# Optimization experiments

Measured on AMD Instinct MI355X. Metric: run time of the kernel, lower is better.

Reference implementation:

```python
import jax, jax.numpy as jnp
import numpy as np

B, T, C, F = 512, 1024, 8, 8
ISIZE = C * F  # 64
OSIZE = 64


def setup_inputs() -> dict:
    key = jax.random.key(0)
    k_x, k_w, k_b = jax.random.split(key, 3)
    x = jax.random.normal(k_x, (B, T, C, F), dtype=jnp.float32)
    # per-group Linear params, torch nn.Linear layout: weight [osize, isize], bias [osize]
    bound = 1.0 / np.sqrt(ISIZE)
    W = jax.random.uniform(k_w, (T, OSIZE, ISIZE), dtype=jnp.float32, minval=-bound, maxval=bound)
    b = jax.random.uniform(k_b, (T, OSIZE), dtype=jnp.float32, minval=-bound, maxval=bound)
    return {"x": x, "W": W, "b": b}


def reference(x, W, b):
    # collapseDims: cat(x.split(1, 2), 3).squeeze(2) == reshape [B,T,C,F] -> [B,T,C*F]
    Bn, Tn, Cn, Fn = x.shape
    xc = x.reshape(Bn, Tn, Cn * Fn)
    # per-slice Linear along dim=1 (T groups): y[b,t,:] = xc[b,t,:] @ W[t].T + b[t]
    out = jnp.einsum("bti,toi->bto", xc, W) + b[None, :, :]
    return out
```

## Files before the change

### kernel.cpp

```cpp
#include <hip/hip_runtime.h>


#define T_DIM 1024
#define B_DIM 512
#define KSZ 64
#define OSZ 64
#define ROWS 64

typedef __attribute__((ext_vector_type(8))) short   short8;
typedef __attribute__((ext_vector_type(8))) unsigned short ushort8;
typedef __attribute__((ext_vector_type(4))) float   f32x4;

static __device__ __forceinline__ unsigned short f2bf(float f) {
    unsigned u = __float_as_uint(f);
    u += 0x7FFFu + ((u >> 16) & 1u);
    return (unsigned short)(u >> 16);
}
static __device__ __forceinline__ float bf2f(unsigned short h) {
    return __uint_as_float((unsigned)h << 16);
}

__global__ __launch_bounds__(256, 4) void pl_kernel(
    const float* __restrict__ x,
    const float* __restrict__ W,
    const float* __restrict__ bias,
    float* __restrict__ out)
{
    __shared__ unsigned short Xh[ROWS * KSZ];
    __shared__ unsigned short Xl[ROWS * KSZ];
    __shared__ unsigned short Wh[OSZ * KSZ];
    __shared__ unsigned short Wl[OSZ * KSZ];

    const int t     = blockIdx.x >> 3;
    const int chunk = blockIdx.x & 7;
    const int row0  = chunk * ROWS;
    const int tid   = threadIdx.x;

    const int sr = tid >> 2;
    const int kc = tid & 3;

    {
        const float* xp = x + ((size_t)(row0 + sr) * T_DIM + t) * KSZ + 16 * kc;
        float4 f0 = *(const float4*)(xp);
        float4 f1 = *(const float4*)(xp + 4);
        float4 f2 = *(const float4*)(xp + 8);
        float4 f3 = *(const float4*)(xp + 12);
        float a[8]  = {f0.x, f0.y, f0.z, f0.w, f1.x, f1.y, f1.z, f1.w};
        float b2[8] = {f2.x, f2.y, f2.z, f2.w, f3.x, f3.y, f3.z, f3.w};
        ushort8 h0, l0, h1, l1;
        #pragma unroll
        for (int j = 0; j < 8; ++j) {
            unsigned short hh = f2bf(a[j]);
            h0[j] = hh; l0[j] = f2bf(a[j] - bf2f(hh));
            unsigned short h2 = f2bf(b2[j]);
            h1[j] = h2; l1[j] = f2bf(b2[j] - bf2f(h2));
        }
        const int p0 = (((2 * kc)     ^ (sr & 7)) << 3);
        const int p1 = (((2 * kc + 1) ^ (sr & 7)) << 3);
        *(ushort8*)&Xh[sr * KSZ + p0] = h0;
        *(ushort8*)&Xl[sr * KSZ + p0] = l0;
        *(ushort8*)&Xh[sr * KSZ + p1] = h1;
        *(ushort8*)&Xl[sr * KSZ + p1] = l1;
    }
    {
        const float* wp = W + (size_t)t * (OSZ * KSZ) + (size_t)sr * KSZ + 16 * kc;
        float4 f0 = *(const float4*)(wp);
        float4 f1 = *(const float4*)(wp + 4);
        float4 f2 = *(const float4*)(wp + 8);
        float4 f3 = *(const float4*)(wp + 12);
        float a[8]  = {f0.x, f0.y, f0.z, f0.w, f1.x, f1.y, f1.z, f1.w};
        float b2[8] = {f2.x, f2.y, f2.z, f2.w, f3.x, f3.y, f3.z, f3.w};
        ushort8 h0, l0, h1, l1;
        #pragma unroll
        for (int j = 0; j < 8; ++j) {
            unsigned short hh = f2bf(a[j]);
            h0[j] = hh; l0[j] = f2bf(a[j] - bf2f(hh));
            unsigned short h2 = f2bf(b2[j]);
            h1[j] = h2; l1[j] = f2bf(b2[j] - bf2f(h2));
        }
        const int p0 = (((2 * kc)     ^ (sr & 7)) << 3);
        const int p1 = (((2 * kc + 1) ^ (sr & 7)) << 3);
        *(ushort8*)&Wh[sr * KSZ + p0] = h0;
        *(ushort8*)&Wl[sr * KSZ + p0] = l0;
        *(ushort8*)&Wh[sr * KSZ + p1] = h1;
        *(ushort8*)&Wl[sr * KSZ + p1] = l1;
    }

    __syncthreads();

    const int w  = tid >> 6;
    const int l  = tid & 63;
    const int kq = l >> 4;

    const int arow = 16 * w + (l & 15);
    short8 ah[2], al[2];
    #pragma unroll
    for (int ks = 0; ks < 2; ++ks) {
        const int kb  = ks * 4 + kq;
        const int pos = (kb ^ (arow & 7)) << 3;
        ah[ks] = *(const short8*)&Xh[arow * KSZ + pos];
        al[ks] = *(const short8*)&Xl[arow * KSZ + pos];
    }

    f32x4 acc[4] = {};
    #pragma unroll
    for (int ct = 0; ct < 4; ++ct) {
        const int brow = 16 * ct + (l & 15);
        #pragma unroll
        for (int ks = 0; ks < 2; ++ks) {
            const int kb  = ks * 4 + kq;
            const int pos = (kb ^ (brow & 7)) << 3;
            short8 bh = *(const short8*)&Wh[brow * KSZ + pos];
            short8 bl = *(const short8*)&Wl[brow * KSZ + pos];
            acc[ct] = __builtin_amdgcn_mfma_f32_16x16x32_bf16(ah[ks], bh, acc[ct], 0, 0, 0);
            acc[ct] = __builtin_amdgcn_mfma_f32_16x16x32_bf16(al[ks], bh, acc[ct], 0, 0, 0);
            acc[ct] = __builtin_amdgcn_mfma_f32_16x16x32_bf16(ah[ks], bl, acc[ct], 0, 0, 0);
        }
    }

    #pragma unroll
    for (int ct = 0; ct < 4; ++ct) {
        const float bv = bias[(size_t)t * OSZ + 16 * ct + (l & 15)];
        #pragma unroll
        for (int j = 0; j < 4; ++j) {
            const size_t b = (size_t)row0 + 16 * w + 4 * kq + j;
            out[(b * T_DIM + t) * OSZ + 16 * ct + (l & 15)] = acc[ct][j] + bv;
        }
    }
}

extern "C" void kernel_launch(void* const* d_in, const int* in_sizes, int n_in,
                              void* d_out, int out_size, void* d_ws, size_t ws_size,
                              hipStream_t stream) {
    const float* x    = (const float*)d_in[0];
    const float* W    = (const float*)d_in[1];
    const float* bias = (const float*)d_in[2];
    float* out        = (float*)d_out;

    dim3 grid(T_DIM * (B_DIM / ROWS));
    dim3 block(256);
    pl_kernel<<<grid, block, 0, stream>>>(x, W, bias, out);
}
```

Before: 72.40 us.

## Process four T slices per block with register-resident weights and LDS-staged coalesced stores

Each block now handles four consecutive t values, with one wave per t. Each wave keeps its own W[t] split into bf16 hi/lo parts in registers instead of staging it in LDS. X rows for four t values are loaded as contiguous 1 KB spans per row. Outputs are staged through a padded LDS buffer so each thread writes 256 contiguous bytes, replacing the previous scattered 64-byte row stores. This improves global coalescing for the strided [B,T,...] layout, at the cost of 68 KB of LDS, lower occupancy (launch bounds 2) and more registers per thread.

```diff
diff --git a/kernel.cpp b/kernel.cpp
--- a/kernel.cpp
+++ b/kernel.cpp
@@ -6,9 +6,10 @@
 #define KSZ 64
 #define OSZ 64
 #define ROWS 64
+#define NT 4
+#define RS 272
 
 typedef __attribute__((ext_vector_type(8))) short   short8;
-typedef __attribute__((ext_vector_type(8))) unsigned short ushort8;
 typedef __attribute__((ext_vector_type(4))) float   f32x4;
 
 static __device__ __forceinline__ unsigned short f2bf(float f) {
@@ -20,112 +21,139 @@
     return __uint_as_float((unsigned)h << 16);
 }
 
-__global__ __launch_bounds__(256, 4) void pl_kernel(
+__global__ __launch_bounds__(256, 2) void pl_kernel(
     const float* __restrict__ x,
     const float* __restrict__ W,
     const float* __restrict__ bias,
     float* __restrict__ out)
 {
-    __shared__ unsigned short Xh[ROWS * KSZ];
-    __shared__ unsigned short Xl[ROWS * KSZ];
-    __shared__ unsigned short Wh[OSZ * KSZ];
-    __shared__ unsigned short Wl[OSZ * KSZ];
+    __shared__ __align__(16) unsigned char smem[69632];
+    unsigned short* Xh = (unsigned short*)smem;
+    unsigned short* Xl = (unsigned short*)(smem + 32768);
+    float* Ob = (float*)smem;
 
-    const int t     = blockIdx.x >> 3;
+    const int quad  = blockIdx.x >> 3;
     const int chunk = blockIdx.x & 7;
+    const int T0    = quad * NT;
     const int row0  = chunk * ROWS;
     const int tid   = threadIdx.x;
+    const int w     = tid >> 6;
+    const int l     = tid & 63;
+    const int n     = l & 15;
+    const int kq    = l >> 4;
 
-    const int sr = tid >> 2;
-    const int kc = tid & 3;
+    short8 wh[4][2], wl[4][2];
+    {
+        const float* wp = W + ((size_t)(T0 + w) * OSZ + n) * KSZ + kq * 8;
+        #pragma unroll
+        for (int ct = 0; ct < 4; ++ct) {
+            #pragma unroll
+            for (int ks = 0; ks < 2; ++ks) {
+                const float* p = wp + (size_t)ct * 16 * KSZ + ks * 32;
+                float4 f0 = *(const float4*)(p);
+                float4 f1 = *(const float4*)(p + 4);
+                float a[8] = {f0.x, f0.y, f0.z, f0.w, f1.x, f1.y, f1.z, f1.w};
+                short8 h, lo;
+                #pragma unroll
+                for (int j = 0; j < 8; ++j) {
+                    unsigned short hh = f2bf(a[j]);
+                    h[j]  = (short)hh;
+                    lo[j] = (short)f2bf(a[j] - bf2f(hh));
+                }
+                wh[ct][ks] = h; wl[ct][ks] = lo;
+            }
+        }
+    }
 
     {
-        const float* xp = x + ((size_t)(row0 + sr) * T_DIM + t) * KSZ + 16 * kc;
-        float4 f0 = *(const float4*)(xp);
-        float4 f1 = *(const float4*)(xp + 4);
-        float4 f2 = *(const float4*)(xp + 8);
-        float4 f3 = *(const float4*)(xp + 12);
-        float a[8]  = {f0.x, f0.y, f0.z, f0.w, f1.x, f1.y, f1.z, f1.w};
-        float b2[8] = {f2.x, f2.y, f2.z, f2.w, f3.x, f3.y, f3.z, f3.w};
-        ushort8 h0, l0, h1, l1;
+        const int sr = tid >> 2;
+        const int sq = tid & 3;
+        const float* xp = x + ((size_t)(row0 + sr) * T_DIM + (T0 + sq)) * KSZ;
+        unsigned short* xh = Xh + sq * 4096 + sr * 64;
+        unsigned short* xl = Xl + sq * 4096 + sr * 64;
+        const int swz = (sr & 7) ^ ((sq & 1) << 2);
         #pragma unroll
-        for (int j = 0; j < 8; ++j) {
-            unsigned short hh = f2bf(a[j]);
-            h0[j] = hh; l0[j] = f2bf(a[j] - bf2f(hh));
-            unsigned short h2 = f2bf(b2[j]);
-            h1[j] = h2; l1[j] = f2bf(b2[j] - bf2f(h2));
+        for (int bb = 0; bb < 4; ++bb) {
+            float4 f0 = *(const float4*)(xp + bb * 16);
+            float4 f1 = *(const float4*)(xp + bb * 16 + 4);
+            float4 f2 = *(const float4*)(xp + bb * 16 + 8);
+            float4 f3 = *(const float4*)(xp + bb * 16 + 12);
+            float a[8]  = {f0.x, f0.y, f0.z, f0.w, f1.x, f1.y, f1.z, f1.w};
+            float b2[8] = {f2.x, f2.y, f2.z, f2.w, f3.x, f3.y, f3.z, f3.w};
+            short8 h0, l0, h1, l1;
+            #pragma unroll
+            for (int j = 0; j < 8; ++j) {
+                unsigned short hh = f2bf(a[j]);
+                h0[j] = (short)hh; l0[j] = (short)f2bf(a[j] - bf2f(hh));
+                unsigned short h2 = f2bf(b2[j]);
+                h1[j] = (short)h2; l1[j] = (short)f2bf(b2[j] - bf2f(h2));
+            }
+            const int g0 = (2 * bb)     ^ swz;
+            const int g1 = (2 * bb + 1) ^ swz;
+            *(short8*)(xh + g0 * 8) = h0;
+            *(short8*)(xl + g0 * 8) = l0;
+            *(short8*)(xh + g1 * 8) = h1;
+            *(short8*)(xl + g1 * 8) = l1;
         }
-        const int p0 = (((2 * kc)     ^ (sr & 7)) << 3);
-        const int p1 = (((2 * kc + 1) ^ (sr & 7)) << 3);
-        *(ushort8*)&Xh[sr * KSZ + p0] = h0;
-        *(ushort8*)&Xl[sr * KSZ + p0] = l0;
-        *(ushort8*)&Xh[sr * KSZ + p1] = h1;
-        *(ushort8*)&Xl[sr * KSZ + p1] = l1;
-    }
-    {
-        const float* wp = W + (size_t)t * (OSZ * KSZ) + (size_t)sr * KSZ + 16 * kc;
-        float4 f0 = *(const float4*)(wp);
-        float4 f1 = *(const float4*)(wp + 4);
-        float4 f2 = *(const float4*)(wp + 8);
-        float4 f3 = *(const float4*)(wp + 12);
-        float a[8]  = {f0.x, f0.y, f0.z, f0.w, f1.x, f1.y, f1.z, f1.w};
-        float b2[8] = {f2.x, f2.y, f2.z, f2.w, f3.x, f3.y, f3.z, f3.w};
-        ushort8 h0, l0, h1, l1;
-        #pragma unroll
-        for (int j = 0; j < 8; ++j) {
-            unsigned short hh = f2bf(a[j]);
-            h0[j] = hh; l0[j] = f2bf(a[j] - bf2f(hh));
-            unsigned short h2 = f2bf(b2[j]);
-            h1[j] = h2; l1[j] = f2bf(b2[j] - bf2f(h2));
-        }
-        const int p0 = (((2 * kc)     ^ (sr & 7)) << 3);
-        const int p1 = (((2 * kc + 1) ^ (sr & 7)) << 3);
-        *(ushort8*)&Wh[sr * KSZ + p0] = h0;
-        *(ushort8*)&Wl[sr * KSZ + p0] = l0;
-        *(ushort8*)&Wh[sr * KSZ + p1] = h1;
-        *(ushort8*)&Wl[sr * KSZ + p1] = l1;
     }
 
     __syncthreads();
 
-    const int w  = tid >> 6;
-    const int l  = tid & 63;
-    const int kq = l >> 4;
-
-    const int arow = 16 * w + (l & 15);
-    short8 ah[2], al[2];
+    short8 ah[4][2], al[4][2];
     #pragma unroll
-    for (int ks = 0; ks < 2; ++ks) {
-        const int kb  = ks * 4 + kq;
-        const int pos = (kb ^ (arow & 7)) << 3;
-        ah[ks] = *(const short8*)&Xh[arow * KSZ + pos];
-        al[ks] = *(const short8*)&Xl[arow * KSZ + pos];
-    }
-
-    f32x4 acc[4] = {};
-    #pragma unroll
-    for (int ct = 0; ct < 4; ++ct) {
-        const int brow = 16 * ct + (l & 15);
+    for (int m = 0; m < 4; ++m) {
+        const int arow = 16 * m + n;
+        const unsigned short* ph = Xh + w * 4096 + arow * 64;
+        const unsigned short* pl = Xl + w * 4096 + arow * 64;
+        const int s2 = (arow & 7) ^ ((w & 1) << 2);
         #pragma unroll
         for (int ks = 0; ks < 2; ++ks) {
-            const int kb  = ks * 4 + kq;
-            const int pos = (kb ^ (brow & 7)) << 3;
-            short8 bh = *(const short8*)&Wh[brow * KSZ + pos];
-            short8 bl = *(const short8*)&Wl[brow * KSZ + pos];
-            acc[ct] = __builtin_amdgcn_mfma_f32_16x16x32_bf16(ah[ks], bh, acc[ct], 0, 0, 0);
-            acc[ct] = __builtin_amdgcn_mfma_f32_16x16x32_bf16(al[ks], bh, acc[ct], 0, 0, 0);
-            acc[ct] = __builtin_amdgcn_mfma_f32_16x16x32_bf16(ah[ks], bl, acc[ct], 0, 0, 0);
+            const int g = (ks * 4 + kq) ^ s2;
+            ah[m][ks] = *(const short8*)(ph + g * 8);
+            al[m][ks] = *(const short8*)(pl + g * 8);
         }
     }
 
+    __syncthreads();
+
+    f32x4 acc[4][4] = {};
     #pragma unroll
-    for (int ct = 0; ct < 4; ++ct) {
-        const float bv = bias[(size_t)t * OSZ + 16 * ct + (l & 15)];
+    for (int m = 0; m < 4; ++m) {
         #pragma unroll
-        for (int j = 0; j < 4; ++j) {
-            const size_t b = (size_t)row0 + 16 * w + 4 * kq + j;
-            out[(b * T_DIM + t) * OSZ + 16 * ct + (l & 15)] = acc[ct][j] + bv;
+        for (int ct = 0; ct < 4; ++ct) {
+            #pragma unroll
+            for (int ks = 0; ks < 2; ++ks) {
+                acc[m][ct] = __builtin_amdgcn_mfma_f32_16x16x32_bf16(ah[m][ks], wh[ct][ks], acc[m][ct], 0, 0, 0);
+                acc[m][ct] = __builtin_amdgcn_mfma_f32_16x16x32_bf16(al[m][ks], wh[ct][ks], acc[m][ct], 0, 0, 0);
+                acc[m][ct] = __builtin_amdgcn_mfma_f32_16x16x32_bf16(ah[m][ks], wl[ct][ks], acc[m][ct], 0, 0, 0);
+            }
         }
+    }
+
+    float bv[4];
+    #pragma unroll
+    for (int ct = 0; ct < 4; ++ct)
+        bv[ct] = bias[(size_t)(T0 + w) * OSZ + 16 * ct + n];
+
+    #pragma unroll
+    for (int m = 0; m < 4; ++m)
+        #pragma unroll
+        for (int ct = 0; ct < 4; ++ct)
+            #pragma unroll
+            for (int j = 0; j < 4; ++j)
+                Ob[(size_t)(16 * m + 4 * kq + j) * RS + w * 68 + 16 * ct + n] =
+                    acc[m][ct][j] + bv[ct];
+
+    __syncthreads();
+
+    {
+        const int sr = tid >> 2;
+        const int sq = tid & 3;
+        const float* src = Ob + (size_t)sr * RS + sq * 68;
+        float* dst = out + ((size_t)(row0 + sr) * T_DIM + (T0 + sq)) * OSZ;
+        #pragma unroll
+        for (int j = 0; j < 16; ++j)
+            *(float4*)(dst + 4 * j) = *(const float4*)(src + 4 * j);
     }
 }
 
@@ -137,7 +165,7 @@
     const float* bias = (const float*)d_in[2];
     float* out        = (float*)d_out;
 
-    dim3 grid(T_DIM * (B_DIM / ROWS));
+    dim3 grid((T_DIM / NT) * (B_DIM / ROWS));
     dim3 block(256);
     pl_kernel<<<grid, block, 0, stream>>>(x, W, bias, out);
 }
```

Result: slower. 97.10 us (+34.1%).

## Pre-split weights to bf16 hi/lo in a separate pass and retile over timesteps

Applied to the files above, without the earlier changes.

A new pre-pass kernel converts W into bf16 high and low halves in the workspace, once per call. The main kernel then reads these bf16 weight fragments straight from global memory into registers rather than staging them through LDS. Each block now covers 4 timesteps by 32 batch rows, one timestep per wave, and block indices are remapped for locality. The old kernel is kept as a fallback when no workspace is available. This cuts per-block weight conversion and LDS traffic, at the cost of an extra launch and workspace reads and writes for W.

```diff
diff --git a/kernel.cpp b/kernel.cpp
--- a/kernel.cpp
+++ b/kernel.cpp
@@ -5,11 +5,11 @@
 #define B_DIM 512
 #define KSZ 64
 #define OSZ 64
-#define ROWS 64
-
-typedef __attribute__((ext_vector_type(8))) short   short8;
-typedef __attribute__((ext_vector_type(8))) unsigned short ushort8;
-typedef __attribute__((ext_vector_type(4))) float   f32x4;
+#define WELEMS (T_DIM * OSZ * KSZ)
+
+typedef __attribute__((ext_vector_type(8))) short short8;
+typedef __attribute__((ext_vector_type(4))) short short4v;
+typedef __attribute__((ext_vector_type(4))) float f32x4;
 
 static __device__ __forceinline__ unsigned short f2bf(float f) {
     unsigned u = __float_as_uint(f);
@@ -20,20 +20,140 @@
     return __uint_as_float((unsigned)h << 16);
 }
 
+
+#define ROWS 32
+#define NT 4
+#define NCHUNK (B_DIM / ROWS)
+
+__global__ __launch_bounds__(256) void w_conv(
+    const float* __restrict__ W, short* __restrict__ ws)
+{
+    const size_t i = ((size_t)blockIdx.x * 256 + threadIdx.x) * 4;
+    float4 w = *(const float4*)(W + i);
+    float a[4] = {w.x, w.y, w.z, w.w};
+    short4v h, lo;
+    #pragma unroll
+    for (int j = 0; j < 4; ++j) {
+        unsigned short hh = f2bf(a[j]);
+        h[j]  = (short)hh;
+        lo[j] = (short)f2bf(a[j] - bf2f(hh));
+    }
+    *(short4v*)(ws + i)          = h;
+    *(short4v*)(ws + WELEMS + i) = lo;
+}
+
 __global__ __launch_bounds__(256, 4) void pl_kernel(
+    const float* __restrict__ x,
+    const short* __restrict__ Wb,
+    const float* __restrict__ bias,
+    float* __restrict__ out)
+{
+    __shared__ short Xh[NT * ROWS * KSZ];
+    __shared__ short Xl[NT * ROWS * KSZ];
+
+    const int orig  = blockIdx.x;
+    const int quad  = (orig & 7) * 32 + (orig >> 7);
+    const int chunk = (orig >> 3) & 15;
+    const int T0    = quad * NT;
+    const int row0  = chunk * ROWS;
+    const int tid   = threadIdx.x;
+    const int ws    = tid >> 6;
+    const int l     = tid & 63;
+    const int n     = l & 15;
+    const int kq    = l >> 4;
+
+    {
+        const int sr   = tid >> 3;
+        const int sq   = (tid >> 1) & 3;
+        const int half = tid & 1;
+        const float* xp = x + ((size_t)(row0 + sr) * T_DIM + (T0 + sq)) * KSZ + 32 * half;
+        short* xh = Xh + sq * (ROWS * KSZ) + sr * KSZ;
+        short* xl = Xl + sq * (ROWS * KSZ) + sr * KSZ;
+        const int swz = (sr & 7) ^ sq;
+        #pragma unroll
+        for (int bb = 0; bb < 4; ++bb) {
+            float4 f0 = *(const float4*)(xp + bb * 8);
+            float4 f1 = *(const float4*)(xp + bb * 8 + 4);
+            float a[8] = {f0.x, f0.y, f0.z, f0.w, f1.x, f1.y, f1.z, f1.w};
+            short8 h, lo;
+            #pragma unroll
+            for (int j = 0; j < 8; ++j) {
+                unsigned short hh = f2bf(a[j]);
+                h[j]  = (short)hh;
+                lo[j] = (short)f2bf(a[j] - bf2f(hh));
+            }
+            const int g = (half * 4 + bb) ^ swz;
+            *(short8*)(xh + g * 8) = h;
+            *(short8*)(xl + g * 8) = lo;
+        }
+    }
+
+    __syncthreads();
+
+    short8 ah[2][2], al[2][2];
+    #pragma unroll
+    for (int m = 0; m < 2; ++m) {
+        const int arow = 16 * m + n;
+        const short* ph = Xh + ws * (ROWS * KSZ) + arow * KSZ;
+        const short* pl = Xl + ws * (ROWS * KSZ) + arow * KSZ;
+        const int s2 = (arow & 7) ^ ws;
+        #pragma unroll
+        for (int ks = 0; ks < 2; ++ks) {
+            const int g = (ks * 4 + kq) ^ s2;
+            ah[m][ks] = *(const short8*)(ph + g * 8);
+            al[m][ks] = *(const short8*)(pl + g * 8);
+        }
+    }
+
+    const int t = T0 + ws;
+    f32x4 acc[2][4] = {};
+    #pragma unroll
+    for (int ct = 0; ct < 4; ++ct) {
+        const size_t wbase = ((size_t)t * OSZ + 16 * ct + n) * KSZ + kq * 8;
+        #pragma unroll
+        for (int ks = 0; ks < 2; ++ks) {
+            short8 wh = *(const short8*)(Wb + wbase + ks * 32);
+            short8 wl = *(const short8*)(Wb + WELEMS + wbase + ks * 32);
+            #pragma unroll
+            for (int m = 0; m < 2; ++m) {
+                acc[m][ct] = __builtin_amdgcn_mfma_f32_16x16x32_bf16(ah[m][ks], wh, acc[m][ct], 0, 0, 0);
+                acc[m][ct] = __builtin_amdgcn_mfma_f32_16x16x32_bf16(al[m][ks], wh, acc[m][ct], 0, 0, 0);
+                acc[m][ct] = __builtin_amdgcn_mfma_f32_16x16x32_bf16(ah[m][ks], wl, acc[m][ct], 0, 0, 0);
+            }
+        }
+    }
+
+    #pragma unroll
+    for (int ct = 0; ct < 4; ++ct) {
+        const float bv = bias[(size_t)t * OSZ + 16 * ct + n];
+        #pragma unroll
+        for (int m = 0; m < 2; ++m) {
+            #pragma unroll
+            for (int j = 0; j < 4; ++j) {
+                const size_t b = (size_t)row0 + 16 * m + 4 * kq + j;
+                out[(b * T_DIM + t) * OSZ + 16 * ct + n] = acc[m][ct][j] + bv;
+            }
+        }
+    }
+}
+
+
+#define FROWS 64
+
+__global__ __launch_bounds__(256, 4) void pl_fallback(
     const float* __restrict__ x,
     const float* __restrict__ W,
     const float* __restrict__ bias,
     float* __restrict__ out)
 {
-    __shared__ unsigned short Xh[ROWS * KSZ];
-    __shared__ unsigned short Xl[ROWS * KSZ];
+    __shared__ unsigned short Xh[FROWS * KSZ];
+    __shared__ unsigned short Xl[FROWS * KSZ];
     __shared__ unsigned short Wh[OSZ * KSZ];
     __shared__ unsigned short Wl[OSZ * KSZ];
 
     const int t     = blockIdx.x >> 3;
     const int chunk = blockIdx.x & 7;
-    const int row0  = chunk * ROWS;
+    const int row0  = chunk * FROWS;
     const int tid   = threadIdx.x;
 
     const int sr = tid >> 2;
@@ -47,7 +167,7 @@
         float4 f3 = *(const float4*)(xp + 12);
         float a[8]  = {f0.x, f0.y, f0.z, f0.w, f1.x, f1.y, f1.z, f1.w};
         float b2[8] = {f2.x, f2.y, f2.z, f2.w, f3.x, f3.y, f3.z, f3.w};
-        ushort8 h0, l0, h1, l1;
+        unsigned short h0[8], l0[8], h1[8], l1[8];
         #pragma unroll
         for (int j = 0; j < 8; ++j) {
             unsigned short hh = f2bf(a[j]);
@@ -57,10 +177,13 @@
         }
         const int p0 = (((2 * kc)     ^ (sr & 7)) << 3);
         const int p1 = (((2 * kc + 1) ^ (sr & 7)) << 3);
-        *(ushort8*)&Xh[sr * KSZ + p0] = h0;
-        *(ushort8*)&Xl[sr * KSZ + p0] = l0;
-        *(ushort8*)&Xh[sr * KSZ + p1] = h1;
-        *(ushort8*)&Xl[sr * KSZ + p1] = l1;
+        #pragma unroll
+        for (int j = 0; j < 8; ++j) {
+            Xh[sr * KSZ + p0 + j] = h0[j];
+            Xl[sr * KSZ + p0 + j] = l0[j];
+            Xh[sr * KSZ + p1 + j] = h1[j];
+            Xl[sr * KSZ + p1 + j] = l1[j];
+        }
     }
     {
         const float* wp = W + (size_t)t * (OSZ * KSZ) + (size_t)sr * KSZ + 16 * kc;
@@ -70,7 +193,7 @@
         float4 f3 = *(const float4*)(wp + 12);
         float a[8]  = {f0.x, f0.y, f0.z, f0.w, f1.x, f1.y, f1.z, f1.w};
         float b2[8] = {f2.x, f2.y, f2.z, f2.w, f3.x, f3.y, f3.z, f3.w};
-        ushort8 h0, l0, h1, l1;
+        unsigned short h0[8], l0[8], h1[8], l1[8];
         #pragma unroll
         for (int j = 0; j < 8; ++j) {
             unsigned short hh = f2bf(a[j]);
@@ -80,10 +203,13 @@
         }
         const int p0 = (((2 * kc)     ^ (sr & 7)) << 3);
         const int p1 = (((2 * kc + 1) ^ (sr & 7)) << 3);
-        *(ushort8*)&Wh[sr * KSZ + p0] = h0;
-        *(ushort8*)&Wl[sr * KSZ + p0] = l0;
-        *(ushort8*)&Wh[sr * KSZ + p1] = h1;
-        *(ushort8*)&Wl[sr * KSZ + p1] = l1;
+        #pragma unroll
+        for (int j = 0; j < 8; ++j) {
+            Wh[sr * KSZ + p0 + j] = h0[j];
+            Wl[sr * KSZ + p0 + j] = l0[j];
+            Wh[sr * KSZ + p1 + j] = h1[j];
+            Wl[sr * KSZ + p1 + j] = l1[j];
+        }
     }
 
     __syncthreads();
@@ -137,7 +263,14 @@
     const float* bias = (const float*)d_in[2];
     float* out        = (float*)d_out;
 
-    dim3 grid(T_DIM * (B_DIM / ROWS));
-    dim3 block(256);
-    pl_kernel<<<grid, block, 0, stream>>>(x, W, bias, out);
-}
+    const size_t need = (size_t)2 * WELEMS * sizeof(short);
+    if (d_ws != nullptr && ws_size >= need) {
+        short* wb = (short*)d_ws;
+        dim3 blk(256);
+        w_conv<<<dim3(WELEMS / (256 * 4)), blk, 0, stream>>>(W, wb);
+        pl_kernel<<<dim3((T_DIM / NT) * NCHUNK), blk, 0, stream>>>(x, wb, bias, out);
+    } else {
+        dim3 blk(256);
+        pl_fallback<<<dim3(T_DIM * (B_DIM / FROWS)), blk, 0, stream>>>(x, W, bias, out);
+    }
+}
```

Result: slower. 97.43 us (+34.6%).

## Process all batch chunks per block with register prefetch, reusing weights

Applied to the files above, without the earlier changes.

Each block now handles one t and loops over all eight 64-row batch chunks. The weight split and bias are loaded once and reused, and the next chunk's x is prefetched into registers while the current chunk is computed. This removes redundant weight loads and conversions, but cuts the grid from 8192 blocks to 1024, which lowers parallelism and the number of waves in flight on a 256-CU device. It also adds per-chunk barriers.

```diff
diff --git a/kernel.cpp b/kernel.cpp
--- a/kernel.cpp
+++ b/kernel.cpp
@@ -6,10 +6,10 @@
 #define KSZ 64
 #define OSZ 64
 #define ROWS 64
+#define NCH (B_DIM / ROWS)
 
-typedef __attribute__((ext_vector_type(8))) short   short8;
-typedef __attribute__((ext_vector_type(8))) unsigned short ushort8;
-typedef __attribute__((ext_vector_type(4))) float   f32x4;
+typedef __attribute__((ext_vector_type(8))) short short8;
+typedef __attribute__((ext_vector_type(4))) float f32x4;
 
 static __device__ __forceinline__ unsigned short f2bf(float f) {
     unsigned u = __float_as_uint(f);
@@ -20,111 +20,133 @@
     return __uint_as_float((unsigned)h << 16);
 }
 
+#define LGKM_BARRIER() do {                                   \
+    asm volatile("s_waitcnt lgkmcnt(0)" ::: "memory");        \
+    __builtin_amdgcn_s_barrier();                             \
+} while (0)
+
 __global__ __launch_bounds__(256, 4) void pl_kernel(
     const float* __restrict__ x,
     const float* __restrict__ W,
     const float* __restrict__ bias,
     float* __restrict__ out)
 {
-    __shared__ unsigned short Xh[ROWS * KSZ];
-    __shared__ unsigned short Xl[ROWS * KSZ];
-    __shared__ unsigned short Wh[OSZ * KSZ];
-    __shared__ unsigned short Wl[OSZ * KSZ];
+    __shared__ short Xh[ROWS * KSZ];
+    __shared__ short Xl[ROWS * KSZ];
+    __shared__ short Wh[OSZ * KSZ];
+    __shared__ short Wl[OSZ * KSZ];
 
-    const int t     = blockIdx.x >> 3;
-    const int chunk = blockIdx.x & 7;
-    const int row0  = chunk * ROWS;
-    const int tid   = threadIdx.x;
+    const int t   = blockIdx.x;
+    const int tid = threadIdx.x;
 
     const int sr = tid >> 2;
     const int kc = tid & 3;
+    const int w  = tid >> 6;
+    const int l  = tid & 63;
+    const int n  = l & 15;
+    const int kq = l >> 4;
+
+    const size_t cstep = (size_t)ROWS * T_DIM * KSZ;
+    const float* xp0 = x + ((size_t)sr * T_DIM + t) * KSZ + 16 * kc;
+
+    float4 pf0 = *(const float4*)(xp0);
+    float4 pf1 = *(const float4*)(xp0 + 4);
+    float4 pf2 = *(const float4*)(xp0 + 8);
+    float4 pf3 = *(const float4*)(xp0 + 12);
 
     {
-        const float* xp = x + ((size_t)(row0 + sr) * T_DIM + t) * KSZ + 16 * kc;
-        float4 f0 = *(const float4*)(xp);
-        float4 f1 = *(const float4*)(xp + 4);
-        float4 f2 = *(const float4*)(xp + 8);
-        float4 f3 = *(const float4*)(xp + 12);
-        float a[8]  = {f0.x, f0.y, f0.z, f0.w, f1.x, f1.y, f1.z, f1.w};
-        float b2[8] = {f2.x, f2.y, f2.z, f2.w, f3.x, f3.y, f3.z, f3.w};
-        ushort8 h0, l0, h1, l1;
+        const float* wp = W + (size_t)t * (OSZ * KSZ) + (size_t)sr * KSZ + 16 * kc;
+        float4 g0 = *(const float4*)(wp);
+        float4 g1 = *(const float4*)(wp + 4);
+        float4 g2 = *(const float4*)(wp + 8);
+        float4 g3 = *(const float4*)(wp + 12);
+        float a[8]  = {g0.x, g0.y, g0.z, g0.w, g1.x, g1.y, g1.z, g1.w};
+        float b2[8] = {g2.x, g2.y, g2.z, g2.w, g3.x, g3.y, g3.z, g3.w};
+        short8 h0, l0, h1, l1;
         #pragma unroll
         for (int j = 0; j < 8; ++j) {
             unsigned short hh = f2bf(a[j]);
-            h0[j] = hh; l0[j] = f2bf(a[j] - bf2f(hh));
+            h0[j] = (short)hh; l0[j] = (short)f2bf(a[j] - bf2f(hh));
             unsigned short h2 = f2bf(b2[j]);
-            h1[j] = h2; l1[j] = f2bf(b2[j] - bf2f(h2));
+            h1[j] = (short)h2; l1[j] = (short)f2bf(b2[j] - bf2f(h2));
         }
         const int p0 = (((2 * kc)     ^ (sr & 7)) << 3);
         const int p1 = (((2 * kc + 1) ^ (sr & 7)) << 3);
-        *(ushort8*)&Xh[sr * KSZ + p0] = h0;
-        *(ushort8*)&Xl[sr * KSZ + p0] = l0;
-        *(ushort8*)&Xh[sr * KSZ + p1] = h1;
-        *(ushort8*)&Xl[sr * KSZ + p1] = l1;
+        *(short8*)&Wh[sr * KSZ + p0] = h0;
+        *(short8*)&Wl[sr * KSZ + p0] = l0;
+        *(short8*)&Wh[sr * KSZ + p1] = h1;
+        *(short8*)&Wl[sr * KSZ + p1] = l1;
     }
-    {
-        const float* wp = W + (size_t)t * (OSZ * KSZ) + (size_t)sr * KSZ + 16 * kc;
-        float4 f0 = *(const float4*)(wp);
-        float4 f1 = *(const float4*)(wp + 4);
-        float4 f2 = *(const float4*)(wp + 8);
-        float4 f3 = *(const float4*)(wp + 12);
-        float a[8]  = {f0.x, f0.y, f0.z, f0.w, f1.x, f1.y, f1.z, f1.w};
-        float b2[8] = {f2.x, f2.y, f2.z, f2.w, f3.x, f3.y, f3.z, f3.w};
-        ushort8 h0, l0, h1, l1;
+
+    float bv[4];
+    #pragma unroll
+    for (int ct = 0; ct < 4; ++ct)
+        bv[ct] = bias[(size_t)t * OSZ + 16 * ct + n];
+
+    const int p0 = (((2 * kc)     ^ (sr & 7)) << 3);
+    const int p1 = (((2 * kc + 1) ^ (sr & 7)) << 3);
+
+    for (int c = 0; c < NCH; ++c) {
+        float a[8]  = {pf0.x, pf0.y, pf0.z, pf0.w, pf1.x, pf1.y, pf1.z, pf1.w};
+        float b2[8] = {pf2.x, pf2.y, pf2.z, pf2.w, pf3.x, pf3.y, pf3.z, pf3.w};
+        short8 h0, l0, h1, l1;
         #pragma unroll
         for (int j = 0; j < 8; ++j) {
             unsigned short hh = f2bf(a[j]);
-            h0[j] = hh; l0[j] = f2bf(a[j] - bf2f(hh));
+            h0[j] = (short)hh; l0[j] = (short)f2bf(a[j] - bf2f(hh));
             unsigned short h2 = f2bf(b2[j]);
-            h1[j] = h2; l1[j] = f2bf(b2[j] - bf2f(h2));
+            h1[j] = (short)h2; l1[j] = (short)f2bf(b2[j] - bf2f(h2));
         }
-        const int p0 = (((2 * kc)     ^ (sr & 7)) << 3);
-        const int p1 = (((2 * kc + 1) ^ (sr & 7)) << 3);
-        *(ushort8*)&Wh[sr * KSZ + p0] = h0;
-        *(ushort8*)&Wl[sr * KSZ + p0] = l0;
-        *(ushort8*)&Wh[sr * KSZ + p1] = h1;
-        *(ushort8*)&Wl[sr * KSZ + p1] = l1;
-    }
 
-    __syncthreads();
+        if (c > 0) LGKM_BARRIER();
 
-    const int w  = tid >> 6;
-    const int l  = tid & 63;
-    const int kq = l >> 4;
+        *(short8*)&Xh[sr * KSZ + p0] = h0;
+        *(short8*)&Xl[sr * KSZ + p0] = l0;
+        *(short8*)&Xh[sr * KSZ + p1] = h1;
+        *(short8*)&Xl[sr * KSZ + p1] = l1;
 
-    const int arow = 16 * w + (l & 15);
-    short8 ah[2], al[2];
-    #pragma unroll
-    for (int ks = 0; ks < 2; ++ks) {
-        const int kb  = ks * 4 + kq;
-        const int pos = (kb ^ (arow & 7)) << 3;
-        ah[ks] = *(const short8*)&Xh[arow * KSZ + pos];
-        al[ks] = *(const short8*)&Xl[arow * KSZ + pos];
-    }
+        if (c + 1 < NCH) {
+            const float* xp = xp0 + (size_t)(c + 1) * cstep;
+            pf0 = *(const float4*)(xp);
+            pf1 = *(const float4*)(xp + 4);
+            pf2 = *(const float4*)(xp + 8);
+            pf3 = *(const float4*)(xp + 12);
+        }
 
-    f32x4 acc[4] = {};
-    #pragma unroll
-    for (int ct = 0; ct < 4; ++ct) {
-        const int brow = 16 * ct + (l & 15);
+        LGKM_BARRIER();
+
+        const int arow = 16 * w + n;
+        short8 ah[2], al[2];
         #pragma unroll
         for (int ks = 0; ks < 2; ++ks) {
-            const int kb  = ks * 4 + kq;
-            const int pos = (kb ^ (brow & 7)) << 3;
-            short8 bh = *(const short8*)&Wh[brow * KSZ + pos];
-            short8 bl = *(const short8*)&Wl[brow * KSZ + pos];
-            acc[ct] = __builtin_amdgcn_mfma_f32_16x16x32_bf16(ah[ks], bh, acc[ct], 0, 0, 0);
-            acc[ct] = __builtin_amdgcn_mfma_f32_16x16x32_bf16(al[ks], bh, acc[ct], 0, 0, 0);
-            acc[ct] = __builtin_amdgcn_mfma_f32_16x16x32_bf16(ah[ks], bl, acc[ct], 0, 0, 0);
+            const int pos = ((ks * 4 + kq) ^ (arow & 7)) << 3;
+            ah[ks] = *(const short8*)&Xh[arow * KSZ + pos];
+            al[ks] = *(const short8*)&Xl[arow * KSZ + pos];
         }
-    }
 
-    #pragma unroll
-    for (int ct = 0; ct < 4; ++ct) {
-        const float bv = bias[(size_t)t * OSZ + 16 * ct + (l & 15)];
+        f32x4 acc[4] = {};
         #pragma unroll
-        for (int j = 0; j < 4; ++j) {
-            const size_t b = (size_t)row0 + 16 * w + 4 * kq + j;
-            out[(b * T_DIM + t) * OSZ + 16 * ct + (l & 15)] = acc[ct][j] + bv;
+        for (int ct = 0; ct < 4; ++ct) {
+            const int brow = 16 * ct + n;
+            #pragma unroll
+            for (int ks = 0; ks < 2; ++ks) {
+                const int pos = ((ks * 4 + kq) ^ (brow & 7)) << 3;
+                short8 bh = *(const short8*)&Wh[brow * KSZ + pos];
+                short8 bl = *(const short8*)&Wl[brow * KSZ + pos];
+                acc[ct] = __builtin_amdgcn_mfma_f32_16x16x32_bf16(ah[ks], bh, acc[ct], 0, 0, 0);
+                acc[ct] = __builtin_amdgcn_mfma_f32_16x16x32_bf16(al[ks], bh, acc[ct], 0, 0, 0);
+                acc[ct] = __builtin_amdgcn_mfma_f32_16x16x32_bf16(ah[ks], bl, acc[ct], 0, 0, 0);
+            }
+        }
+
+        const int row0 = c * ROWS;
+        #pragma unroll
+        for (int ct = 0; ct < 4; ++ct) {
+            #pragma unroll
+            for (int j = 0; j < 4; ++j) {
+                const size_t b = (size_t)row0 + 16 * w + 4 * kq + j;
+                out[(b * T_DIM + t) * OSZ + 16 * ct + n] = acc[ct][j] + bv[ct];
+            }
         }
     }
 }
@@ -137,7 +159,7 @@
     const float* bias = (const float*)d_in[2];
     float* out        = (float*)d_out;
 
-    dim3 grid(T_DIM * (B_DIM / ROWS));
+    dim3 grid(T_DIM);
     dim3 block(256);
     pl_kernel<<<grid, block, 0, stream>>>(x, W, bias, out);
 }
```

Result: faster. 64.42 us (-11.0%).
